# Kernel optimization log

Measured on AMD Instinct MI355X. Metric: run time of the kernel, lower is better.

## Reference

```python
import jax, jax.numpy as jnp
import numpy as np

BATCH, H, NFAM = 32768, 1024, 10


def setup_inputs() -> dict:
    key = jax.random.key(0)
    k1, k2, k3, k4 = jax.random.split(key, 4)
    scale1 = 1.0 / np.sqrt(2 * H)
    scale2 = 1.0 / np.sqrt(H)
    return {
        "features": jax.random.normal(k1, (BATCH, H), dtype=jnp.float32),
        "prototypes": jax.random.normal(k2, (NFAM, H), dtype=jnp.float32),
        "W1": jax.random.normal(k3, (2 * H, H), dtype=jnp.float32) * scale1,
        "b1": jnp.zeros((H,), dtype=jnp.float32),
        "W2": jax.random.normal(k4, (H, H), dtype=jnp.float32) * scale2,
        "b2": jnp.zeros((H,), dtype=jnp.float32),
    }


def reference(features, prototypes, W1, b1, W2, b2):
    # Squared euclidean distances via the norm trick (avoids [B, NFAM, H] blowup).
    # argmin over squared distances == argmin over cdist (sqrt is monotone).
    f2 = jnp.sum(features * features, axis=1, keepdims=True)        # [B, 1]
    p2 = jnp.sum(prototypes * prototypes, axis=1)                   # [NFAM]
    d2 = f2 + p2[None, :] - 2.0 * (features @ prototypes.T)         # [B, NFAM]
    nearest_idx = jnp.argmin(d2, axis=1)                            # [B]
    nearest_prototypes = prototypes[nearest_idx]                    # [B, H]
    combined = jnp.concatenate([features, nearest_prototypes], axis=1)  # [B, 2H]
    hidden = jax.nn.relu(combined @ W1 + b1)                        # [B, H]
    adapted = hidden @ W2 + b2                                      # [B, H]
    return adapted
```

## Files before the change

### kernel.cpp

```cpp
#include <hip/hip_runtime.h>
#include <stdint.h>
#include <stddef.h>

#define BATCH 32768
#define HDIM  1024
#define NFAM  10

typedef short bf16x8 __attribute__((ext_vector_type(8)));
typedef float f32x4  __attribute__((ext_vector_type(4)));

__device__ __forceinline__ unsigned short f2bf(float x) {
  unsigned int u = __builtin_bit_cast(unsigned int, x);
  u += 0x7fffu + ((u >> 16) & 1u);
  return (unsigned short)(u >> 16);
}

__device__ __forceinline__ void async_cp16(unsigned short* lds_dst, const unsigned short* g_src) {
  __builtin_amdgcn_global_load_lds(
      (const __attribute__((address_space(1))) unsigned int*)g_src,
      (__attribute__((address_space(3))) unsigned int*)lds_dst,
      16, 0, 0);
}

__global__ __launch_bounds__(256) void transpose_cast(
    const float* __restrict__ in, unsigned short* __restrict__ out, int R, int C) {
  __shared__ float tile[64][65];
  const int t = threadIdx.x;
  const int c = t & 63;
  const int r0 = t >> 6;
  const int rbase = blockIdx.y * 64, cbase = blockIdx.x * 64;
#pragma unroll
  for (int i = 0; i < 16; ++i) {
    int r = r0 + i * 4;
    tile[r][c] = in[(size_t)(rbase + r) * C + cbase + c];
  }
  __syncthreads();
#pragma unroll
  for (int i = 0; i < 16; ++i) {
    int r = r0 + i * 4;
    out[(size_t)(cbase + r) * R + rbase + c] = f2bf(tile[c][r]);
  }
}

__global__ __launch_bounds__(256) void proto_prep(
    const float* __restrict__ protos, float* __restrict__ p2) {
  __shared__ float red[4];
  const int j = blockIdx.x, t = threadIdx.x;
  float4 v = ((const float4*)(protos + (size_t)j * HDIM))[t];
  float s = v.x * v.x + v.y * v.y + v.z * v.z + v.w * v.w;
#pragma unroll
  for (int o = 32; o > 0; o >>= 1) s += __shfl_down(s, o);
  if ((t & 63) == 0) red[t >> 6] = s;
  __syncthreads();
  if (t == 0) p2[j] = red[0] + red[1] + red[2] + red[3];
}

__global__ __launch_bounds__(256) void proto_contrib(
    const float* __restrict__ protos, const float* __restrict__ W1,
    const float* __restrict__ b1, float* __restrict__ protoC) {
  const int j = blockIdx.y;
  const int n = blockIdx.x * 256 + threadIdx.x;
  const float* w = W1 + (size_t)HDIM * HDIM + n;
  const float* p = protos + (size_t)j * HDIM;
  float s0 = 0.f, s1 = 0.f, s2 = 0.f, s3 = 0.f;
#pragma unroll 4
  for (int k = 0; k < HDIM; k += 4) {
    s0 += p[k]     * w[(size_t)k * HDIM];
    s1 += p[k + 1] * w[(size_t)(k + 1) * HDIM];
    s2 += p[k + 2] * w[(size_t)(k + 2) * HDIM];
    s3 += p[k + 3] * w[(size_t)(k + 3) * HDIM];
  }
  protoC[j * HDIM + n] = (s0 + s1) + (s2 + s3) + b1[n];
}

__global__ __launch_bounds__(256) void nearest_kernel(
    const float* __restrict__ feats, const float* __restrict__ protos,
    const float* __restrict__ p2, unsigned short* __restrict__ featsB,
    int* __restrict__ idx) {
  __shared__ float pl[NFAM * HDIM];
  const int t = threadIdx.x;
#pragma unroll
  for (int j = 0; j < NFAM; ++j)
    ((float4*)pl)[t + 256 * j] = ((const float4*)protos)[t + 256 * j];
  __syncthreads();

  const int wave = t >> 6, lane = t & 63;
  float P2[NFAM];
#pragma unroll
  for (int j = 0; j < NFAM; ++j) P2[j] = p2[j];

#pragma unroll
  for (int rr = 0; rr < 4; ++rr) {
    const int row = blockIdx.x * 16 + wave * 4 + rr;
    const float* f = feats + (size_t)row * HDIM;

    float dot[NFAM];
#pragma unroll
    for (int j = 0; j < NFAM; ++j) dot[j] = 0.f;
    float f2 = 0.f;

#pragma unroll
    for (int ch = 0; ch < 4; ++ch) {
      const int k4 = ch * 64 + lane;
      float4 v = ((const float4*)f)[k4];
      f2 += v.x * v.x + v.y * v.y + v.z * v.z + v.w * v.w;
#pragma unroll
      for (int j = 0; j < NFAM; ++j) {
        float4 p = ((const float4*)pl)[j * 256 + k4];
        dot[j] += v.x * p.x + v.y * p.y + v.z * p.z + v.w * p.w;
      }
      uint2 pk;
      pk.x = (unsigned)f2bf(v.x) | ((unsigned)f2bf(v.y) << 16);
      pk.y = (unsigned)f2bf(v.z) | ((unsigned)f2bf(v.w) << 16);
      *(uint2*)(featsB + (size_t)row * HDIM + k4 * 4) = pk;
    }

#pragma unroll
    for (int o = 32; o > 0; o >>= 1) {
      f2 += __shfl_down(f2, o);
#pragma unroll
      for (int j = 0; j < NFAM; ++j) dot[j] += __shfl_down(dot[j], o);
    }
    if (lane == 0) {
      int best = 0;
      float bd = f2 + P2[0] - 2.f * dot[0];
#pragma unroll
      for (int j = 1; j < NFAM; ++j) {
        float d = f2 + P2[j] - 2.f * dot[j];
        if (d < bd) { bd = d; best = j; }
      }
      idx[row] = best;
    }
  }
}

template <int EPI>
__global__ __launch_bounds__(256) void gemm_kernel(
    const unsigned short* __restrict__ A,
    const unsigned short* __restrict__ Bt,
    const int* __restrict__ idx,
    const float* __restrict__ protoC,
    const float* __restrict__ bias,
    unsigned short* __restrict__ outB,
    float* __restrict__ outF) {
  constexpr int K = 1024;
  __shared__ unsigned short ldsA[2][128 * 32];
  __shared__ unsigned short ldsB[2][128 * 32];
  __shared__ int idxLds[128];

  const int t    = threadIdx.x;
  const int lane = t & 63;
  const int wid  = t >> 6;
  const int quad = lane >> 4;
  const int r16  = lane & 15;

  const int b = blockIdx.x;
  const int rowBase = ((b >> 6) * 8 + (b & 7)) * 128;
  const int colBase = ((b >> 3) & 7) * 128;
  const int wm = (wid >> 1) * 64;
  const int wn = (wid & 1) * 64;

  if (EPI) {
    if (t < 128) idxLds[t] = idx[rowBase + t];
    __syncthreads();
  }

  f32x4 acc[4][4];
#pragma unroll
  for (int i = 0; i < 4; ++i)
#pragma unroll
    for (int j = 0; j < 4; ++j) acc[i][j] = (f32x4){0.f, 0.f, 0.f, 0.f};

  const int r0 = t >> 2, r1 = r0 + 64;
  const int q = (t & 3) ^ ((t >> 3) & 3);
  const unsigned short* aBase0 = A + (size_t)(rowBase + r0) * K + q * 8;
  const unsigned short* aBase1 = A + (size_t)(rowBase + r1) * K + q * 8;
  const unsigned short* bB0 = Bt + (size_t)(colBase + r0) * K + q * 8;
  const unsigned short* bB1 = Bt + (size_t)(colBase + r1) * K + q * 8;

  const int pr = quad ^ ((r16 >> 1) & 3);

  for (int kb = 0; kb < K; kb += 64) {
#pragma unroll
    for (int s = 0; s < 2; ++s) {
      async_cp16(&ldsA[s][t * 8],         aBase0 + kb + s * 32);
      async_cp16(&ldsA[s][(t + 256) * 8], aBase1 + kb + s * 32);
      async_cp16(&ldsB[s][t * 8],         bB0 + kb + s * 32);
      async_cp16(&ldsB[s][(t + 256) * 8], bB1 + kb + s * 32);
    }
    __syncthreads();

#pragma unroll
    for (int s = 0; s < 2; ++s) {
      bf16x8 af[4], bfr[4];
#pragma unroll
      for (int mi = 0; mi < 4; ++mi)
        af[mi] = *(const bf16x8*)(&ldsA[s][(wm + mi * 16 + r16) * 32 + pr * 8]);
#pragma unroll
      for (int ni = 0; ni < 4; ++ni)
        bfr[ni] = *(const bf16x8*)(&ldsB[s][(wn + ni * 16 + r16) * 32 + pr * 8]);
#pragma unroll
      for (int mi = 0; mi < 4; ++mi)
#pragma unroll
        for (int ni = 0; ni < 4; ++ni)
          acc[mi][ni] = __builtin_amdgcn_mfma_f32_16x16x32_bf16(af[mi], bfr[ni], acc[mi][ni], 0, 0, 0);
    }
    __syncthreads();
  }

#pragma unroll
  for (int mi = 0; mi < 4; ++mi) {
    const int lrow0 = wm + mi * 16 + quad * 4;
    int pid[4];
    if (EPI) {
#pragma unroll
      for (int r = 0; r < 4; ++r) pid[r] = idxLds[lrow0 + r];
    }
#pragma unroll
    for (int ni = 0; ni < 4; ++ni) {
      const int grow0 = rowBase + lrow0;
      const int gcol  = colBase + wn + ni * 16 + r16;
      if (EPI) {
#pragma unroll
        for (int r = 0; r < 4; ++r) {
          float v = acc[mi][ni][r] + protoC[(size_t)pid[r] * HDIM + gcol];
          v = fmaxf(v, 0.0f);
          outB[(size_t)(grow0 + r) * 1024 + gcol] = f2bf(v);
        }
      } else {
        const float bv = bias[gcol];
#pragma unroll
        for (int r = 0; r < 4; ++r)
          outF[(size_t)(grow0 + r) * 1024 + gcol] = acc[mi][ni][r] + bv;
      }
    }
  }
}

extern "C" void kernel_launch(void* const* d_in, const int* in_sizes, int n_in,
                              void* d_out, int out_size, void* d_ws, size_t ws_size,
                              hipStream_t stream) {
  const float* feats  = (const float*)d_in[0];
  const float* protos = (const float*)d_in[1];
  const float* W1     = (const float*)d_in[2];
  const float* b1     = (const float*)d_in[3];
  const float* W2     = (const float*)d_in[4];
  const float* b2     = (const float*)d_in[5];
  float* out = (float*)d_out;

  unsigned short* featsB  = (unsigned short*)d_ws;
  unsigned short* hiddenB = featsB + (size_t)BATCH * HDIM;
  unsigned short* W1t     = hiddenB + (size_t)BATCH * HDIM;
  unsigned short* W2t     = W1t + (size_t)HDIM * HDIM;
  float* protoC = (float*)(W2t + (size_t)HDIM * HDIM);
  float* p2     = protoC + NFAM * HDIM;
  int* idx      = (int*)(p2 + NFAM + 2);

  transpose_cast<<<dim3(HDIM / 64, HDIM / 64), 256, 0, stream>>>(W1, W1t, HDIM, HDIM);
  transpose_cast<<<dim3(HDIM / 64, HDIM / 64), 256, 0, stream>>>(W2, W2t, HDIM, HDIM);
  proto_prep<<<NFAM, 256, 0, stream>>>(protos, p2);
  proto_contrib<<<dim3(HDIM / 256, NFAM), 256, 0, stream>>>(protos, W1, b1, protoC);
  nearest_kernel<<<BATCH / 16, 256, 0, stream>>>(feats, protos, p2, featsB, idx);
  gemm_kernel<1><<<2048, 256, 0, stream>>>(featsB, W1t, idx, protoC, nullptr, hiddenB, nullptr);
  gemm_kernel<0><<<2048, 256, 0, stream>>>(hiddenB, W2t, nullptr, nullptr, b2, nullptr, out);
}
```

Baseline: 450.6 us.

## Double-buffer GEMM LDS tiles with async prefetch and split-K proto_contrib

The GEMM main loop now uses two LDS buffers. It issues the async global-to-LDS copies for the next K tile before computing the current one and waits with an explicit vmcnt, so load latency overlaps MFMA work. The idx staging through LDS is dropped in favour of direct global reads in the epilogue. proto_contrib is split along K across four waves with an LDS reduction, launching 4x more blocks to expose more parallelism. The cost is doubled LDS use per block (64KB), which may reduce occupancy, and the manual waitcnt/barrier scheduling is fragile.

```diff
diff --git a/kernel.cpp b/kernel.cpp
--- a/kernel.cpp
+++ b/kernel.cpp
@@ -58,19 +58,21 @@
 __global__ __launch_bounds__(256) void proto_contrib(
     const float* __restrict__ protos, const float* __restrict__ W1,
     const float* __restrict__ b1, float* __restrict__ protoC) {
-  const int j = blockIdx.y;
-  const int n = blockIdx.x * 256 + threadIdx.x;
-  const float* w = W1 + (size_t)HDIM * HDIM + n;
-  const float* p = protos + (size_t)j * HDIM;
-  float s0 = 0.f, s1 = 0.f, s2 = 0.f, s3 = 0.f;
-#pragma unroll 4
-  for (int k = 0; k < HDIM; k += 4) {
-    s0 += p[k]     * w[(size_t)k * HDIM];
-    s1 += p[k + 1] * w[(size_t)(k + 1) * HDIM];
-    s2 += p[k + 2] * w[(size_t)(k + 2) * HDIM];
-    s3 += p[k + 3] * w[(size_t)(k + 3) * HDIM];
-  }
-  protoC[j * HDIM + n] = (s0 + s1) + (s2 + s3) + b1[n];
+  __shared__ float red[4][64];
+  const int j  = blockIdx.y;
+  const int ln = threadIdx.x & 63;
+  const int ks = threadIdx.x >> 6;
+  const int n  = blockIdx.x * 64 + ln;
+  const float* p = protos + (size_t)j * HDIM + ks * 256;
+  const float* w = W1 + (size_t)(HDIM + ks * 256) * HDIM + n;
+  float s = 0.f;
+#pragma unroll 16
+  for (int kk = 0; kk < 256; ++kk)
+    s += p[kk] * w[(size_t)kk * HDIM];
+  red[ks][ln] = s;
+  __syncthreads();
+  if (ks == 0)
+    protoC[j * HDIM + n] = red[0][ln] + red[1][ln] + red[2][ln] + red[3][ln] + b1[n];
 }
 
 __global__ __launch_bounds__(256) void nearest_kernel(
@@ -144,9 +146,8 @@
     unsigned short* __restrict__ outB,
     float* __restrict__ outF) {
   constexpr int K = 1024;
-  __shared__ unsigned short ldsA[2][128 * 32];
-  __shared__ unsigned short ldsB[2][128 * 32];
-  __shared__ int idxLds[128];
+  __shared__ unsigned short ldsA[2][2][128 * 32];
+  __shared__ unsigned short ldsB[2][2][128 * 32];
 
   const int t    = threadIdx.x;
   const int lane = t & 63;
@@ -159,11 +160,6 @@
   const int colBase = ((b >> 3) & 7) * 128;
   const int wm = (wid >> 1) * 64;
   const int wn = (wid & 1) * 64;
-
-  if (EPI) {
-    if (t < 128) idxLds[t] = idx[rowBase + t];
-    __syncthreads();
-  }
 
   f32x4 acc[4][4];
 #pragma unroll
@@ -180,46 +176,63 @@
 
   const int pr = quad ^ ((r16 >> 1) & 3);
 
+#define ISSUE_TILE(buf, kb)                                        \
+  {                                                                \
+    _Pragma("unroll")                                              \
+    for (int s = 0; s < 2; ++s) {                                  \
+      async_cp16(&ldsA[buf][s][t * 8],         aBase0 + (kb) + s * 32); \
+      async_cp16(&ldsA[buf][s][(t + 256) * 8], aBase1 + (kb) + s * 32); \
+      async_cp16(&ldsB[buf][s][t * 8],         bB0 + (kb) + s * 32);    \
+      async_cp16(&ldsB[buf][s][(t + 256) * 8], bB1 + (kb) + s * 32);    \
+    }                                                              \
+  }
+
+  ISSUE_TILE(0, 0);
+  int cur = 0;
   for (int kb = 0; kb < K; kb += 64) {
-#pragma unroll
-    for (int s = 0; s < 2; ++s) {
-      async_cp16(&ldsA[s][t * 8],         aBase0 + kb + s * 32);
-      async_cp16(&ldsA[s][(t + 256) * 8], aBase1 + kb + s * 32);
-      async_cp16(&ldsB[s][t * 8],         bB0 + kb + s * 32);
-      async_cp16(&ldsB[s][(t + 256) * 8], bB1 + kb + s * 32);
-    }
-    __syncthreads();
+    if (kb + 64 < K) {
+      ISSUE_TILE(cur ^ 1, kb + 64);
+      asm volatile("s_waitcnt vmcnt(8)" ::: "memory");
+    } else {
+      asm volatile("s_waitcnt vmcnt(0)" ::: "memory");
+    }
+    __builtin_amdgcn_s_barrier();
+    __builtin_amdgcn_sched_barrier(0);
 
 #pragma unroll
     for (int s = 0; s < 2; ++s) {
       bf16x8 af[4], bfr[4];
 #pragma unroll
       for (int mi = 0; mi < 4; ++mi)
-        af[mi] = *(const bf16x8*)(&ldsA[s][(wm + mi * 16 + r16) * 32 + pr * 8]);
+        af[mi] = *(const bf16x8*)(&ldsA[cur][s][(wm + mi * 16 + r16) * 32 + pr * 8]);
 #pragma unroll
       for (int ni = 0; ni < 4; ++ni)
-        bfr[ni] = *(const bf16x8*)(&ldsB[s][(wn + ni * 16 + r16) * 32 + pr * 8]);
+        bfr[ni] = *(const bf16x8*)(&ldsB[cur][s][(wn + ni * 16 + r16) * 32 + pr * 8]);
 #pragma unroll
       for (int mi = 0; mi < 4; ++mi)
 #pragma unroll
         for (int ni = 0; ni < 4; ++ni)
           acc[mi][ni] = __builtin_amdgcn_mfma_f32_16x16x32_bf16(af[mi], bfr[ni], acc[mi][ni], 0, 0, 0);
     }
-    __syncthreads();
-  }
+
+    __builtin_amdgcn_sched_barrier(0);
+    __builtin_amdgcn_s_barrier();
+    cur ^= 1;
+  }
+#undef ISSUE_TILE
 
 #pragma unroll
   for (int mi = 0; mi < 4; ++mi) {
     const int lrow0 = wm + mi * 16 + quad * 4;
+    const int grow0 = rowBase + lrow0;
     int pid[4];
     if (EPI) {
 #pragma unroll
-      for (int r = 0; r < 4; ++r) pid[r] = idxLds[lrow0 + r];
+      for (int r = 0; r < 4; ++r) pid[r] = idx[grow0 + r];
     }
 #pragma unroll
     for (int ni = 0; ni < 4; ++ni) {
-      const int grow0 = rowBase + lrow0;
-      const int gcol  = colBase + wn + ni * 16 + r16;
+      const int gcol = colBase + wn + ni * 16 + r16;
       if (EPI) {
 #pragma unroll
         for (int r = 0; r < 4; ++r) {
@@ -259,7 +272,7 @@
   transpose_cast<<<dim3(HDIM / 64, HDIM / 64), 256, 0, stream>>>(W1, W1t, HDIM, HDIM);
   transpose_cast<<<dim3(HDIM / 64, HDIM / 64), 256, 0, stream>>>(W2, W2t, HDIM, HDIM);
   proto_prep<<<NFAM, 256, 0, stream>>>(protos, p2);
-  proto_contrib<<<dim3(HDIM / 256, NFAM), 256, 0, stream>>>(protos, W1, b1, protoC);
+  proto_contrib<<<dim3(HDIM / 64, NFAM), 256, 0, stream>>>(protos, W1, b1, protoC);
   nearest_kernel<<<BATCH / 16, 256, 0, stream>>>(feats, protos, p2, featsB, idx);
   gemm_kernel<1><<<2048, 256, 0, stream>>>(featsB, W1t, idx, protoC, nullptr, hiddenB, nullptr);
   gemm_kernel<0><<<2048, 256, 0, stream>>>(hiddenB, W2t, nullptr, nullptr, b2, nullptr, out);
```

Result: faster. 429.8 us (-4.6%).
